# Kernel optimization log

Hardware: AMD Instinct MI355X
Metric: run time of the kernel (lower is better)

## Reference

```python
import jax, jax.numpy as jnp
import numpy as np

B, T_IN, T_OUT = 256, 256, 32
E, H, Y, V = 512, 1024, 1024, 32000


def gru_cell(x, h, Wih, Whh, bih, bhh):
    # torch GRU gate order: r, z, n
    gi = x @ Wih.T + bih
    gh = h @ Whh.T + bhh
    ir, iz, inn = jnp.split(gi, 3, axis=-1)
    hr, hz, hn = jnp.split(gh, 3, axis=-1)
    r = jax.nn.sigmoid(ir + hr)
    z = jax.nn.sigmoid(iz + hz)
    n = jnp.tanh(inn + r * hn)
    return (1.0 - z) * n + z * h


def setup_inputs() -> dict:
    key = jax.random.key(0)
    ks = jax.random.split(key, 32)
    s = 0.05
    p = lambda k, shape: (jax.random.normal(k, shape, jnp.float32) * s)
    inp = {
        'x': jax.random.randint(ks[0], (B, T_IN), 0, V),
        'y': (jax.random.uniform(ks[1], (B, T_OUT, Y)) < 0.01).astype(jnp.float32),
        'emb': p(ks[2], (V, E)),
        # encoder layer 0 (input E) and layer 1 (input H)
        'enc_Wih0': p(ks[3], (3 * H, E)), 'enc_Whh0': p(ks[4], (3 * H, H)),
        'enc_bih0': p(ks[5], (3 * H,)), 'enc_bhh0': p(ks[6], (3 * H,)),
        'enc_Wih1': p(ks[7], (3 * H, H)), 'enc_Whh1': p(ks[8], (3 * H, H)),
        'enc_bih1': p(ks[9], (3 * H,)), 'enc_bhh1': p(ks[10], (3 * H,)),
        # decoder layer 0 (input Y) and layer 1 (input H)
        'dec_Wih0': p(ks[11], (3 * H, Y)), 'dec_Whh0': p(ks[12], (3 * H, H)),
        'dec_bih0': p(ks[13], (3 * H,)), 'dec_bhh0': p(ks[14], (3 * H,)),
        'dec_Wih1': p(ks[15], (3 * H, H)), 'dec_Whh1': p(ks[16], (3 * H, H)),
        'dec_bih1': p(ks[17], (3 * H,)), 'dec_bhh1': p(ks[18], (3 * H,)),
        # mapping: Linear(2H -> Y) followed by log-softmax
        'map_W': p(ks[19], (Y, 2 * H)), 'map_b': p(ks[20], (Y,)),
    }
    return inp


def reference(x, y, emb,
              enc_Wih0, enc_Whh0, enc_bih0, enc_bhh0,
              enc_Wih1, enc_Whh1, enc_bih1, enc_bhh1,
              dec_Wih0, dec_Whh0, dec_bih0, dec_bhh0,
              dec_Wih1, dec_Whh1, dec_bih1, dec_bhh1,
              map_W, map_b):
    batch = x.shape[0]
    h_dim = enc_Whh0.shape[1]

    # ---- encoder: 2-layer GRU over seq_in, h0 = 0 ----
    seq = emb[x].transpose(1, 0, 2)  # [T_in, B, E]
    finals = []
    for prm in ((enc_Wih0, enc_Whh0, enc_bih0, enc_bhh0),
                (enc_Wih1, enc_Whh1, enc_bih1, enc_bhh1)):
        def step(h, xt, prm=prm):
            hn = gru_cell(xt, h, *prm)
            return hn, hn
        hT, seq = jax.lax.scan(step, jnp.zeros((batch, h_dim), seq.dtype), seq)
        finals.append(hT)
    enc_out = seq.transpose(1, 0, 2)  # [B, T_in, H]

    # ---- decoder: teacher-forced, one step at a time ----
    y_shift = jnp.concatenate([jnp.zeros((batch, 1, y.shape[2]), y.dtype), y[:, :-1]], axis=1)
    ys_in = y_shift.transpose(1, 0, 2)  # [T_out, B, Y]
    ys_t = y.transpose(1, 0, 2)         # [T_out, B, Y]
    dec0 = (dec_Wih0, dec_Whh0, dec_bih0, dec_bhh0)
    dec1 = (dec_Wih1, dec_Whh1, dec_bih1, dec_bhh1)

    def dec_step(carry, inp):
        h1, h2 = carry
        y_in, y_t = inp
        h1 = gru_cell(y_in, h1, *dec0)
        h2 = gru_cell(h1, h2, *dec1)           # dec_out == top-layer hidden
        scores = jnp.einsum('bsh,bh->bs', enc_out, h2)
        alpha = jax.nn.softmax(scores, axis=-1)          # over encoder positions
        attn = jnp.einsum('bsh,bs->bh', enc_out, alpha)  # [B, H]
        logits = jnp.concatenate([attn, h2], axis=1) @ map_W.T + map_b
        logp = jax.nn.log_softmax(logits, axis=-1)
        loss_t = -(logp * y_t).sum()
        return (h1, h2), loss_t

    _, losses = jax.lax.scan(dec_step, (finals[0], finals[1]), (ys_in, ys_t))
    return losses.sum() / y.sum()
```

## Files before the change

kernel.cpp:

```cpp
#include <hip/hip_runtime.h>
#include <hip/hip_bf16.h>
#include <math.h>

#define BATCH 256
#define T_IN 256
#define T_OUT 32
#define E_DIM 512
#define H_DIM 1024
#define Y_DIM 1024
#define G_DIM 3072

typedef __attribute__((ext_vector_type(8))) __bf16 bf16x8;
typedef __attribute__((ext_vector_type(4))) float f32x4;
typedef __attribute__((ext_vector_type(4))) unsigned int u32x4;

__device__ __forceinline__ unsigned short f2bf_raw(float x) {
    unsigned int u = __builtin_bit_cast(unsigned int, x);
    u += 0x7FFFu + ((u >> 16) & 1u);
    return (unsigned short)(u >> 16);
}

__global__ __launch_bounds__(256) void f32_to_bf16(
    const float* __restrict__ src, short* __restrict__ dst, int n4)
{
    for (int i = blockIdx.x * 256 + threadIdx.x; i < n4; i += gridDim.x * 256) {
        float4 f = *(const float4*)(src + 4 * (size_t)i);
        short4 o;
        o.x = (short)f2bf_raw(f.x);
        o.y = (short)f2bf_raw(f.y);
        o.z = (short)f2bf_raw(f.z);
        o.w = (short)f2bf_raw(f.w);
        *(short4*)(dst + 4 * (size_t)i) = o;
    }
}

__global__ __launch_bounds__(256) void gemm_bf(
    const short* __restrict__ Ab0, const float* __restrict__ Af0,
    const int* __restrict__ g0, int gs0, int lda0, int K0,
    const short* __restrict__ W0, const float* __restrict__ b0, float* __restrict__ C0,
    const short* __restrict__ Ab1, const float* __restrict__ Af1,
    int lda1, int K1,
    const short* __restrict__ W1, const float* __restrict__ b1, float* __restrict__ C1,
    int N)
{
    const int z = blockIdx.z;
    const short* Ab = z ? Ab1 : Ab0;
    const float* Af = z ? Af1 : Af0;
    const int* gat = z ? nullptr : g0;
    const int gs = z ? 1 : gs0;
    const int lda = z ? lda1 : lda0;
    const int K = z ? K1 : K0;
    const short* W = z ? W1 : W0;
    const float* bias = z ? b1 : b0;
    float* C = z ? C1 : C0;

    __shared__ __align__(16) short As[64 * 40];
    __shared__ __align__(16) short Ws[64 * 40];

    const int tid = threadIdx.x;
    const int bm = blockIdx.x * 64;
    const int bn = blockIdx.y * 64;

    const int srow = tid >> 2;
    const int sch = tid & 3;

    const short* abase = nullptr;
    const float* afbase = nullptr;
    if (Ab) {
        int ridx = gat ? gat[(size_t)(bm + srow) * gs] : (bm + srow);
        abase = Ab + (size_t)ridx * lda;
    } else if (Af) {
        int ridx = gat ? gat[(size_t)(bm + srow) * gs] : (bm + srow);
        afbase = Af + (size_t)ridx * lda;
    }
    const short* wbase = W + (size_t)(bn + srow) * K;

    short* asdst = &As[srow * 40 + sch * 8];
    short* wsdst = &Ws[srow * 40 + sch * 8];

    const int w = tid >> 6;
    const int lane = tid & 63;
    const int wm = (w >> 1) * 32;
    const int wn = (w & 1) * 32;
    const int lrow = lane & 15;
    const int lko = (lane >> 4) * 8;

    const short* ar0 = &As[(wm + lrow) * 40 + lko];
    const short* ar1 = &As[(wm + 16 + lrow) * 40 + lko];
    const short* br0 = &Ws[(wn + lrow) * 40 + lko];
    const short* br1 = &Ws[(wn + 16 + lrow) * 40 + lko];

    f32x4 acc00 = {0.f, 0.f, 0.f, 0.f};
    f32x4 acc01 = acc00, acc10 = acc00, acc11 = acc00;

    for (int k0 = 0; k0 < K; k0 += 32) {
        u32x4 av;
        if (abase) {
            av = *(const u32x4*)(abase + k0 + sch * 8);
        } else if (afbase) {
            const float* fp = afbase + k0 + sch * 8;
            float4 f0 = *(const float4*)(fp);
            float4 f1 = *(const float4*)(fp + 4);
            av.x = ((unsigned)f2bf_raw(f0.y) << 16) | f2bf_raw(f0.x);
            av.y = ((unsigned)f2bf_raw(f0.w) << 16) | f2bf_raw(f0.z);
            av.z = ((unsigned)f2bf_raw(f1.y) << 16) | f2bf_raw(f1.x);
            av.w = ((unsigned)f2bf_raw(f1.w) << 16) | f2bf_raw(f1.z);
        } else {
            av.x = av.y = av.z = av.w = 0u;
        }
        u32x4 wv = *(const u32x4*)(wbase + k0 + sch * 8);
        *(u32x4*)asdst = av;
        *(u32x4*)wsdst = wv;
        __syncthreads();

        bf16x8 a0 = __builtin_bit_cast(bf16x8, *(const u32x4*)ar0);
        bf16x8 a1 = __builtin_bit_cast(bf16x8, *(const u32x4*)ar1);
        bf16x8 b0v = __builtin_bit_cast(bf16x8, *(const u32x4*)br0);
        bf16x8 b1v = __builtin_bit_cast(bf16x8, *(const u32x4*)br1);

        acc00 = __builtin_amdgcn_mfma_f32_16x16x32_bf16(a0, b0v, acc00, 0, 0, 0);
        acc01 = __builtin_amdgcn_mfma_f32_16x16x32_bf16(a0, b1v, acc01, 0, 0, 0);
        acc10 = __builtin_amdgcn_mfma_f32_16x16x32_bf16(a1, b0v, acc10, 0, 0, 0);
        acc11 = __builtin_amdgcn_mfma_f32_16x16x32_bf16(a1, b1v, acc11, 0, 0, 0);

        __syncthreads();
    }

    const int rbase = (lane >> 4) * 4;
    const int cl = lane & 15;
    #pragma unroll
    for (int fm = 0; fm < 2; ++fm) {
        #pragma unroll
        for (int fn = 0; fn < 2; ++fn) {
            f32x4 a = fm ? (fn ? acc11 : acc10) : (fn ? acc01 : acc00);
            int col = bn + wn + fn * 16 + cl;
            float bv = bias[col];
            #pragma unroll
            for (int j = 0; j < 4; ++j) {
                int row = bm + wm + fm * 16 + rbase + j;
                C[(size_t)row * N + col] = a[j] + bv;
            }
        }
    }
}

__global__ __launch_bounds__(256) void gru_fuse(
    const float* __restrict__ gi, const float* __restrict__ gh,
    const float* __restrict__ h, float* __restrict__ hout,
    short* __restrict__ hbf, short* __restrict__ copy_out)
{
    int i = blockIdx.x * 256 + threadIdx.x;
    int b = i >> 10;
    int j = i & 1023;
    const float* gib = gi + (size_t)b * G_DIM;
    const float* ghb = gh + (size_t)b * G_DIM;
    float ir = gib[j], iz = gib[H_DIM + j], in_ = gib[2 * H_DIM + j];
    float hr = ghb[j], hz = ghb[H_DIM + j], hn = ghb[2 * H_DIM + j];
    float r = 1.f / (1.f + expf(-(ir + hr)));
    float zz = 1.f / (1.f + expf(-(iz + hz)));
    float n = tanhf(in_ + r * hn);
    float hv = h[i];
    float o = (1.f - zz) * n + zz * hv;
    hout[i] = o;
    short ob = (short)f2bf_raw(o);
    hbf[i] = ob;
    if (copy_out) copy_out[i] = ob;
}

__global__ __launch_bounds__(256) void attn_scores(
    const short* __restrict__ enc, const float* __restrict__ h2,
    float* __restrict__ scores)
{
    int wid = (blockIdx.x * 256 + threadIdx.x) >> 6;
    int lane = threadIdx.x & 63;
    int s = wid >> 8;
    int b = wid & 255;
    const unsigned int* e2 =
        (const unsigned int*)(enc + ((size_t)s * BATCH + b) * H_DIM);
    const float* hb = h2 + (size_t)b * H_DIM;
    float sum = 0.f;
    #pragma unroll
    for (int p = lane; p < H_DIM / 2; p += 64) {
        unsigned int u = e2[p];
        float lo = __builtin_bit_cast(float, u << 16);
        float hi = __builtin_bit_cast(float, u & 0xFFFF0000u);
        sum += lo * hb[2 * p] + hi * hb[2 * p + 1];
    }
    for (int off = 32; off; off >>= 1) sum += __shfl_down(sum, off);
    if (!lane) scores[(size_t)b * T_IN + s] = sum;
}

__global__ __launch_bounds__(256) void softmax_rows(float* __restrict__ scores)
{
    int b = blockIdx.x, t = threadIdx.x;
    float v = scores[(size_t)b * T_IN + t];
    int lane = t & 63, w = t >> 6;
    float m = v;
    for (int off = 32; off; off >>= 1) m = fmaxf(m, __shfl_down(m, off));
    __shared__ float r1[4];
    if (!lane) r1[w] = m;
    __syncthreads();
    m = fmaxf(fmaxf(r1[0], r1[1]), fmaxf(r1[2], r1[3]));
    float ex = expf(v - m);
    float s = ex;
    for (int off = 32; off; off >>= 1) s += __shfl_down(s, off);
    __shared__ float r2[4];
    if (!lane) r2[w] = s;
    __syncthreads();
    s = r2[0] + r2[1] + r2[2] + r2[3];
    scores[(size_t)b * T_IN + t] = ex / s;
}

__global__ __launch_bounds__(256) void attn_apply(
    const short* __restrict__ enc, const float* __restrict__ alpha,
    float* __restrict__ attn)
{
    int b = blockIdx.x, t = threadIdx.x;
    float acc[4] = {0.f, 0.f, 0.f, 0.f};
    for (int s = 0; s < T_IN; ++s) {
        float a = alpha[(size_t)b * T_IN + s];
        const short* e = enc + ((size_t)s * BATCH + b) * H_DIM;
        #pragma unroll
        for (int i = 0; i < 4; ++i) {
            unsigned int u = ((unsigned int)(unsigned short)e[t + i * 256]) << 16;
            acc[i] += a * __builtin_bit_cast(float, u);
        }
    }
    #pragma unroll
    for (int i = 0; i < 4; ++i) attn[(size_t)b * H_DIM + t + i * 256] = acc[i];
}

__global__ __launch_bounds__(256) void concat_kernel(
    const float* __restrict__ attn, const float* __restrict__ h2,
    short* __restrict__ cat)
{
    int i = blockIdx.x * 256 + threadIdx.x;
    int b = i >> 11;
    int j = i & 2047;
    float v = (j < H_DIM) ? attn[(size_t)b * H_DIM + j]
                          : h2[(size_t)b * H_DIM + j - H_DIM];
    cat[i] = (short)f2bf_raw(v);
}

__global__ __launch_bounds__(256) void loss_kernel(
    const float* __restrict__ logits, const float* __restrict__ yt,
    float* __restrict__ loss_acc)
{
    int b = blockIdx.x, t = threadIdx.x;
    const float* lrow = logits + (size_t)b * Y_DIM;
    float l[4];
    #pragma unroll
    for (int i = 0; i < 4; ++i) l[i] = lrow[t + i * 256];
    float m = fmaxf(fmaxf(l[0], l[1]), fmaxf(l[2], l[3]));
    int lane = t & 63, w = t >> 6;
    for (int off = 32; off; off >>= 1) m = fmaxf(m, __shfl_down(m, off));
    __shared__ float sm[4];
    if (!lane) sm[w] = m;
    __syncthreads();
    m = fmaxf(fmaxf(sm[0], sm[1]), fmaxf(sm[2], sm[3]));
    float es = 0.f;
    #pragma unroll
    for (int i = 0; i < 4; ++i) es += expf(l[i] - m);
    for (int off = 32; off; off >>= 1) es += __shfl_down(es, off);
    __shared__ float ss[4];
    if (!lane) ss[w] = es;
    __syncthreads();
    float sum = ss[0] + ss[1] + ss[2] + ss[3];
    float logZ = m + logf(sum);
    const float* yrow = yt + (size_t)b * (T_OUT * Y_DIM);
    float part = 0.f;
    #pragma unroll
    for (int i = 0; i < 4; ++i) part += yrow[t + i * 256] * (logZ - l[i]);
    for (int off = 32; off; off >>= 1) part += __shfl_down(part, off);
    __shared__ float sp[4];
    if (!lane) sp[w] = part;
    __syncthreads();
    if (t == 0) atomicAdd(loss_acc, sp[0] + sp[1] + sp[2] + sp[3]);
}

__global__ __launch_bounds__(256) void ysum_kernel(
    const float* __restrict__ y, float* __restrict__ ysum, int n)
{
    float s = 0.f;
    for (int i = blockIdx.x * 256 + threadIdx.x; i < n; i += gridDim.x * 256)
        s += y[i];
    int lane = threadIdx.x & 63, w = threadIdx.x >> 6;
    for (int off = 32; off; off >>= 1) s += __shfl_down(s, off);
    __shared__ float sw[4];
    if (!lane) sw[w] = s;
    __syncthreads();
    if (!threadIdx.x) atomicAdd(ysum, sw[0] + sw[1] + sw[2] + sw[3]);
}

__global__ __launch_bounds__(256) void init_kernel(
    float* __restrict__ h0, float* __restrict__ h1,
    short* __restrict__ h0bf, short* __restrict__ h1bf,
    float* __restrict__ loss, float* __restrict__ ysum)
{
    int i = blockIdx.x * 256 + threadIdx.x;
    if (i < BATCH * H_DIM) {
        h0[i] = 0.f; h1[i] = 0.f; h0bf[i] = 0; h1bf[i] = 0;
    }
    if (i == 0) { *loss = 0.f; *ysum = 0.f; }
}

__global__ void final_kernel(const float* __restrict__ loss,
                             const float* __restrict__ ysum,
                             float* __restrict__ out)
{
    if (threadIdx.x == 0) out[0] = loss[0] / ysum[0];
}

extern "C" void kernel_launch(void* const* d_in, const int* in_sizes, int n_in,
                              void* d_out, int out_size, void* d_ws, size_t ws_size,
                              hipStream_t stream)
{
    const int*   x     = (const int*)d_in[0];
    const float* y     = (const float*)d_in[1];
    const float* emb   = (const float*)d_in[2];
    const float* eWih0 = (const float*)d_in[3];
    const float* eWhh0 = (const float*)d_in[4];
    const float* ebih0 = (const float*)d_in[5];
    const float* ebhh0 = (const float*)d_in[6];
    const float* eWih1 = (const float*)d_in[7];
    const float* eWhh1 = (const float*)d_in[8];
    const float* ebih1 = (const float*)d_in[9];
    const float* ebhh1 = (const float*)d_in[10];
    const float* dWih0 = (const float*)d_in[11];
    const float* dWhh0 = (const float*)d_in[12];
    const float* dbih0 = (const float*)d_in[13];
    const float* dbhh0 = (const float*)d_in[14];
    const float* dWih1 = (const float*)d_in[15];
    const float* dWhh1 = (const float*)d_in[16];
    const float* dbih1 = (const float*)d_in[17];
    const float* dbhh1 = (const float*)d_in[18];
    const float* mapW  = (const float*)d_in[19];
    const float* mapb  = (const float*)d_in[20];
    float* out = (float*)d_out;

    char* p = (char*)d_ws;
    short* enc_bf = (short*)p;               p += (size_t)T_IN * BATCH * H_DIM * 2;
    short* eWih0b = (short*)p;               p += (size_t)G_DIM * E_DIM * 2;
    short* eWhh0b = (short*)p;               p += (size_t)G_DIM * H_DIM * 2;
    short* eWih1b = (short*)p;               p += (size_t)G_DIM * H_DIM * 2;
    short* eWhh1b = (short*)p;               p += (size_t)G_DIM * H_DIM * 2;
    short* dWih0b = (short*)p;               p += (size_t)G_DIM * Y_DIM * 2;
    short* dWhh0b = (short*)p;               p += (size_t)G_DIM * H_DIM * 2;
    short* dWih1b = (short*)p;               p += (size_t)G_DIM * H_DIM * 2;
    short* dWhh1b = (short*)p;               p += (size_t)G_DIM * H_DIM * 2;
    short* mapWb  = (short*)p;               p += (size_t)Y_DIM * 2 * H_DIM * 2;
    float* gi0 = (float*)p;                  p += (size_t)BATCH * G_DIM * 4;
    float* gh0 = (float*)p;                  p += (size_t)BATCH * G_DIM * 4;
    float* gi1 = (float*)p;                  p += (size_t)BATCH * G_DIM * 4;
    float* gh1 = (float*)p;                  p += (size_t)BATCH * G_DIM * 4;
    float* h0  = (float*)p;                  p += (size_t)BATCH * H_DIM * 4;
    float* h1  = (float*)p;                  p += (size_t)BATCH * H_DIM * 4;
    short* h0bf = (short*)p;                 p += (size_t)BATCH * H_DIM * 2;
    short* h1bf = (short*)p;                 p += (size_t)BATCH * H_DIM * 2;
    float* scores = (float*)p;               p += (size_t)BATCH * T_IN * 4;
    float* attn   = (float*)p;               p += (size_t)BATCH * H_DIM * 4;
    short* cat_bf = (short*)p;               p += (size_t)BATCH * 2 * H_DIM * 2;
    float* logits = (float*)p;               p += (size_t)BATCH * Y_DIM * 4;
    float* loss_acc = (float*)p;             p += 8;
    float* ysum = loss_acc + 1;

    dim3 blk(256);

    f32_to_bf16<<<dim3(512), blk, 0, stream>>>(eWih0, eWih0b, G_DIM * E_DIM / 4);
    f32_to_bf16<<<dim3(512), blk, 0, stream>>>(eWhh0, eWhh0b, G_DIM * H_DIM / 4);
    f32_to_bf16<<<dim3(512), blk, 0, stream>>>(eWih1, eWih1b, G_DIM * H_DIM / 4);
    f32_to_bf16<<<dim3(512), blk, 0, stream>>>(eWhh1, eWhh1b, G_DIM * H_DIM / 4);
    f32_to_bf16<<<dim3(512), blk, 0, stream>>>(dWih0, dWih0b, G_DIM * Y_DIM / 4);
    f32_to_bf16<<<dim3(512), blk, 0, stream>>>(dWhh0, dWhh0b, G_DIM * H_DIM / 4);
    f32_to_bf16<<<dim3(512), blk, 0, stream>>>(dWih1, dWih1b, G_DIM * H_DIM / 4);
    f32_to_bf16<<<dim3(512), blk, 0, stream>>>(dWhh1, dWhh1b, G_DIM * H_DIM / 4);
    f32_to_bf16<<<dim3(512), blk, 0, stream>>>(mapW, mapWb, Y_DIM * 2 * H_DIM / 4);

    init_kernel<<<dim3(1024), blk, 0, stream>>>(h0, h1, h0bf, h1bf, loss_acc, ysum);
    ysum_kernel<<<dim3(2048), blk, 0, stream>>>(y, ysum, BATCH * T_OUT * Y_DIM);

    dim3 gGate(BATCH / 64, G_DIM / 64, 2);

    for (int t = 0; t < T_IN; ++t) {
        gemm_bf<<<gGate, blk, 0, stream>>>(
            nullptr, emb, x + t, T_IN, E_DIM, E_DIM, eWih0b, ebih0, gi0,
            h0bf, nullptr, H_DIM, H_DIM, eWhh0b, ebhh0, gh0, G_DIM);
        gru_fuse<<<dim3(1024), blk, 0, stream>>>(gi0, gh0, h0, h0, h0bf, nullptr);
        gemm_bf<<<gGate, blk, 0, stream>>>(
            h0bf, nullptr, nullptr, 1, H_DIM, H_DIM, eWih1b, ebih1, gi1,
            h1bf, nullptr, H_DIM, H_DIM, eWhh1b, ebhh1, gh1, G_DIM);
        gru_fuse<<<dim3(1024), blk, 0, stream>>>(
            gi1, gh1, h1, h1, h1bf, enc_bf + (size_t)t * BATCH * H_DIM);
    }

    for (int t = 0; t < T_OUT; ++t) {
        const float* yin = (t == 0) ? nullptr : (y + (size_t)(t - 1) * Y_DIM);
        gemm_bf<<<gGate, blk, 0, stream>>>(
            nullptr, yin, nullptr, 1, T_OUT * Y_DIM, Y_DIM, dWih0b, dbih0, gi0,
            h0bf, nullptr, H_DIM, H_DIM, dWhh0b, dbhh0, gh0, G_DIM);
        gru_fuse<<<dim3(1024), blk, 0, stream>>>(gi0, gh0, h0, h0, h0bf, nullptr);
        gemm_bf<<<gGate, blk, 0, stream>>>(
            h0bf, nullptr, nullptr, 1, H_DIM, H_DIM, dWih1b, dbih1, gi1,
            h1bf, nullptr, H_DIM, H_DIM, dWhh1b, dbhh1, gh1, G_DIM);
        gru_fuse<<<dim3(1024), blk, 0, stream>>>(gi1, gh1, h1, h1, h1bf, nullptr);

        attn_scores<<<dim3(T_IN * BATCH / 4), blk, 0, stream>>>(enc_bf, h1, scores);
        softmax_rows<<<dim3(BATCH), blk, 0, stream>>>(scores);
        attn_apply<<<dim3(BATCH), blk, 0, stream>>>(enc_bf, scores, attn);
        concat_kernel<<<dim3(2048), blk, 0, stream>>>(attn, h1, cat_bf);

        dim3 gMap(BATCH / 64, Y_DIM / 64, 1);
        gemm_bf<<<gMap, blk, 0, stream>>>(
            cat_bf, nullptr, nullptr, 1, 2 * H_DIM, 2 * H_DIM, mapWb, mapb, logits,
            nullptr, nullptr, 0, 0, nullptr, nullptr, nullptr, Y_DIM);
        loss_kernel<<<dim3(BATCH), blk, 0, stream>>>(
            logits, y + (size_t)t * Y_DIM, loss_acc);
    }

    final_kernel<<<dim3(1), dim3(64), 0, stream>>>(loss_acc, ysum, out);
}
```

Measured before the change: 15.23 ms.

## Fuse GRU gate GEMMs with cell update, wavefront-pipeline layers, batch decoder attention

```diff
diff --git a/kernel.cpp b/kernel.cpp
--- a/kernel.cpp
+++ b/kernel.cpp
@@ -18,6 +18,16 @@
     unsigned int u = __builtin_bit_cast(unsigned int, x);
     u += 0x7FFFu + ((u >> 16) & 1u);
     return (unsigned short)(u >> 16);
+}
+__device__ __forceinline__ float bf2f(short s) {
+    unsigned int u = ((unsigned int)(unsigned short)s) << 16;
+    return __builtin_bit_cast(float, u);
+}
+__device__ __forceinline__ f32x4 mfma16(bf16x8 a, bf16x8 b, f32x4 c) {
+    return __builtin_amdgcn_mfma_f32_16x16x32_bf16(a, b, c, 0, 0, 0);
+}
+__device__ __forceinline__ bf16x8 ldsb8(const short* p) {
+    return __builtin_bit_cast(bf16x8, *(const u32x4*)p);
 }
 
 __global__ __launch_bounds__(256) void f32_to_bf16(
@@ -34,166 +44,179 @@
     }
 }
 
-__global__ __launch_bounds__(256) void gemm_bf(
-    const short* __restrict__ Ab0, const float* __restrict__ Af0,
-    const int* __restrict__ g0, int gs0, int lda0, int K0,
-    const short* __restrict__ W0, const float* __restrict__ b0, float* __restrict__ C0,
-    const short* __restrict__ Ab1, const float* __restrict__ Af1,
-    int lda1, int K1,
-    const short* __restrict__ W1, const float* __restrict__ b1, float* __restrict__ C1,
-    int N)
-{
-    const int z = blockIdx.z;
-    const short* Ab = z ? Ab1 : Ab0;
-    const float* Af = z ? Af1 : Af0;
-    const int* gat = z ? nullptr : g0;
-    const int gs = z ? 1 : gs0;
-    const int lda = z ? lda1 : lda0;
-    const int K = z ? K1 : K0;
-    const short* W = z ? W1 : W0;
-    const float* bias = z ? b1 : b0;
-    float* C = z ? C1 : C0;
-
-    __shared__ __align__(16) short As[64 * 40];
-    __shared__ __align__(16) short Ws[64 * 40];
+struct CellArgs {
+    const float* Af; const short* Ab; const int* gat; int gs; int lda; int Kx;
+    const short* Wih; const short* Whh;
+    const float* bih; const float* bhh;
+    const short* hbf;
+    const float* hf;
+    float* houtf; short* houtbf; short* copy;
+    int active;
+};
+
+__global__ __launch_bounds__(256) void cell_kernel(CellArgs cA, CellArgs cB)
+{
+    const CellArgs a = blockIdx.z ? cB : cA;
+    if (!a.active) return;
+
+    __shared__ __align__(16) short As[2 * 1280];
+    __shared__ __align__(16) short Ws[6 * 2560];
 
     const int tid = threadIdx.x;
-    const int bm = blockIdx.x * 64;
+    const int bm = blockIdx.x * 32;
     const int bn = blockIdx.y * 64;
 
-    const int srow = tid >> 2;
-    const int sch = tid & 3;
-
-    const short* abase = nullptr;
-    const float* afbase = nullptr;
-    if (Ab) {
-        int ridx = gat ? gat[(size_t)(bm + srow) * gs] : (bm + srow);
-        abase = Ab + (size_t)ridx * lda;
-    } else if (Af) {
-        int ridx = gat ? gat[(size_t)(bm + srow) * gs] : (bm + srow);
-        afbase = Af + (size_t)ridx * lda;
-    }
-    const short* wbase = W + (size_t)(bn + srow) * K;
-
-    short* asdst = &As[srow * 40 + sch * 8];
-    short* wsdst = &Ws[srow * 40 + sch * 8];
-
+    const int sr = (tid >> 2) & 31;
+    const int ss = tid >> 7;
+    const int wr = tid >> 2;
+    const int ch = (tid & 3) * 8;
+
+    const float* axf = nullptr;
+    const short* axb = nullptr;
+    if (a.Af) {
+        int ridx = a.gat ? a.gat[(size_t)(bm + sr) * a.gs] : (bm + sr);
+        axf = a.Af + (size_t)ridx * a.lda + ch;
+    } else if (a.Ab) {
+        axb = a.Ab + (size_t)(bm + sr) * a.lda + ch;
+    }
+    const short* ahb = a.hbf + (size_t)(bm + sr) * H_DIM + ch;
+
+    const short* wsrc[6];
+    #pragma unroll
+    for (int g = 0; g < 3; ++g) {
+        wsrc[g]     = a.Wih + (size_t)(g * H_DIM + bn + wr) * a.Kx + ch;
+        wsrc[g + 3] = a.Whh + (size_t)(g * H_DIM + bn + wr) * H_DIM + ch;
+    }
+    short* adst  = &As[ss * 1280 + sr * 40 + ch];
+    short* wdst0 = &Ws[wr * 40 + ch];
+
+    const int lane = tid & 63;
     const int w = tid >> 6;
-    const int lane = tid & 63;
-    const int wm = (w >> 1) * 32;
-    const int wn = (w & 1) * 32;
-    const int lrow = lane & 15;
-    const int lko = (lane >> 4) * 8;
-
-    const short* ar0 = &As[(wm + lrow) * 40 + lko];
-    const short* ar1 = &As[(wm + 16 + lrow) * 40 + lko];
-    const short* br0 = &Ws[(wn + lrow) * 40 + lko];
-    const short* br1 = &Ws[(wn + 16 + lrow) * 40 + lko];
-
-    f32x4 acc00 = {0.f, 0.f, 0.f, 0.f};
-    f32x4 acc01 = acc00, acc10 = acc00, acc11 = acc00;
-
-    for (int k0 = 0; k0 < K; k0 += 32) {
-        u32x4 av;
-        if (abase) {
-            av = *(const u32x4*)(abase + k0 + sch * 8);
-        } else if (afbase) {
-            const float* fp = afbase + k0 + sch * 8;
-            float4 f0 = *(const float4*)(fp);
-            float4 f1 = *(const float4*)(fp + 4);
-            av.x = ((unsigned)f2bf_raw(f0.y) << 16) | f2bf_raw(f0.x);
-            av.y = ((unsigned)f2bf_raw(f0.w) << 16) | f2bf_raw(f0.z);
-            av.z = ((unsigned)f2bf_raw(f1.y) << 16) | f2bf_raw(f1.x);
-            av.w = ((unsigned)f2bf_raw(f1.w) << 16) | f2bf_raw(f1.z);
-        } else {
-            av.x = av.y = av.z = av.w = 0u;
-        }
-        u32x4 wv = *(const u32x4*)(wbase + k0 + sch * 8);
-        *(u32x4*)asdst = av;
-        *(u32x4*)wsdst = wv;
+    const int lr = lane & 15;
+    const int ko = (lane >> 4) * 8;
+    const short* pax0 = &As[lr * 40 + ko];
+    const short* pax1 = &As[(16 + lr) * 40 + ko];
+    const short* pah0 = &As[1280 + lr * 40 + ko];
+    const short* pah1 = &As[1280 + (16 + lr) * 40 + ko];
+    const int wc = (w * 16 + lr) * 40 + ko;
+
+    f32x4 accI[3][2] = {{{0.f,0.f,0.f,0.f}}};
+    f32x4 accH[3][2] = {{{0.f,0.f,0.f,0.f}}};
+
+    const int Kx = a.Kx;
+    for (int k0 = 0; k0 < H_DIM; k0 += 32) {
+        const bool xact = (k0 < Kx);
+        u32x4 av = {0u, 0u, 0u, 0u};
+        if (ss) {
+            av = *(const u32x4*)(ahb + k0);
+        } else if (xact) {
+            if (axb) {
+                av = *(const u32x4*)(axb + k0);
+            } else if (axf) {
+                float4 f0 = *(const float4*)(axf + k0);
+                float4 f1 = *(const float4*)(axf + k0 + 4);
+                av.x = ((unsigned)f2bf_raw(f0.y) << 16) | f2bf_raw(f0.x);
+                av.y = ((unsigned)f2bf_raw(f0.w) << 16) | f2bf_raw(f0.z);
+                av.z = ((unsigned)f2bf_raw(f1.y) << 16) | f2bf_raw(f1.x);
+                av.w = ((unsigned)f2bf_raw(f1.w) << 16) | f2bf_raw(f1.z);
+            }
+        }
+        if (ss || xact) *(u32x4*)adst = av;
+        #pragma unroll
+        for (int i = 0; i < 6; ++i) {
+            if (i >= 3 || xact)
+                *(u32x4*)(wdst0 + i * 2560) = *(const u32x4*)(wsrc[i] + k0);
+        }
         __syncthreads();
-
-        bf16x8 a0 = __builtin_bit_cast(bf16x8, *(const u32x4*)ar0);
-        bf16x8 a1 = __builtin_bit_cast(bf16x8, *(const u32x4*)ar1);
-        bf16x8 b0v = __builtin_bit_cast(bf16x8, *(const u32x4*)br0);
-        bf16x8 b1v = __builtin_bit_cast(bf16x8, *(const u32x4*)br1);
-
-        acc00 = __builtin_amdgcn_mfma_f32_16x16x32_bf16(a0, b0v, acc00, 0, 0, 0);
-        acc01 = __builtin_amdgcn_mfma_f32_16x16x32_bf16(a0, b1v, acc01, 0, 0, 0);
-        acc10 = __builtin_amdgcn_mfma_f32_16x16x32_bf16(a1, b0v, acc10, 0, 0, 0);
-        acc11 = __builtin_amdgcn_mfma_f32_16x16x32_bf16(a1, b1v, acc11, 0, 0, 0);
-
+        bf16x8 ah0 = ldsb8(pah0), ah1 = ldsb8(pah1);
+        #pragma unroll
+        for (int g = 0; g < 3; ++g) {
+            bf16x8 wh = ldsb8(&Ws[(g + 3) * 2560 + wc]);
+            accH[g][0] = mfma16(ah0, wh, accH[g][0]);
+            accH[g][1] = mfma16(ah1, wh, accH[g][1]);
+        }
+        if (xact) {
+            bf16x8 ax0 = ldsb8(pax0), ax1 = ldsb8(pax1);
+            #pragma unroll
+            for (int g = 0; g < 3; ++g) {
+                bf16x8 wi = ldsb8(&Ws[g * 2560 + wc]);
+                accI[g][0] = mfma16(ax0, wi, accI[g][0]);
+                accI[g][1] = mfma16(ax1, wi, accI[g][1]);
+            }
+        }
         __syncthreads();
     }
 
-    const int rbase = (lane >> 4) * 4;
-    const int cl = lane & 15;
-    #pragma unroll
-    for (int fm = 0; fm < 2; ++fm) {
-        #pragma unroll
-        for (int fn = 0; fn < 2; ++fn) {
-            f32x4 a = fm ? (fn ? acc11 : acc10) : (fn ? acc01 : acc00);
-            int col = bn + wn + fn * 16 + cl;
-            float bv = bias[col];
-            #pragma unroll
-            for (int j = 0; j < 4; ++j) {
-                int row = bm + wm + fm * 16 + rbase + j;
-                C[(size_t)row * N + col] = a[j] + bv;
-            }
-        }
-    }
-}
-
-__global__ __launch_bounds__(256) void gru_fuse(
-    const float* __restrict__ gi, const float* __restrict__ gh,
-    const float* __restrict__ h, float* __restrict__ hout,
-    short* __restrict__ hbf, short* __restrict__ copy_out)
-{
-    int i = blockIdx.x * 256 + threadIdx.x;
-    int b = i >> 10;
-    int j = i & 1023;
-    const float* gib = gi + (size_t)b * G_DIM;
-    const float* ghb = gh + (size_t)b * G_DIM;
-    float ir = gib[j], iz = gib[H_DIM + j], in_ = gib[2 * H_DIM + j];
-    float hr = ghb[j], hz = ghb[H_DIM + j], hn = ghb[2 * H_DIM + j];
-    float r = 1.f / (1.f + expf(-(ir + hr)));
-    float zz = 1.f / (1.f + expf(-(iz + hz)));
-    float n = tanhf(in_ + r * hn);
-    float hv = h[i];
-    float o = (1.f - zz) * n + zz * hv;
-    hout[i] = o;
-    short ob = (short)f2bf_raw(o);
-    hbf[i] = ob;
-    if (copy_out) copy_out[i] = ob;
-}
-
-__global__ __launch_bounds__(256) void attn_scores(
-    const short* __restrict__ enc, const float* __restrict__ h2,
-    float* __restrict__ scores)
-{
-    int wid = (blockIdx.x * 256 + threadIdx.x) >> 6;
-    int lane = threadIdx.x & 63;
-    int s = wid >> 8;
-    int b = wid & 255;
-    const unsigned int* e2 =
-        (const unsigned int*)(enc + ((size_t)s * BATCH + b) * H_DIM);
-    const float* hb = h2 + (size_t)b * H_DIM;
-    float sum = 0.f;
-    #pragma unroll
-    for (int p = lane; p < H_DIM / 2; p += 64) {
-        unsigned int u = e2[p];
-        float lo = __builtin_bit_cast(float, u << 16);
-        float hi = __builtin_bit_cast(float, u & 0xFFFF0000u);
-        sum += lo * hb[2 * p] + hi * hb[2 * p + 1];
-    }
-    for (int off = 32; off; off >>= 1) sum += __shfl_down(sum, off);
-    if (!lane) scores[(size_t)b * T_IN + s] = sum;
-}
-
-__global__ __launch_bounds__(256) void softmax_rows(float* __restrict__ scores)
-{
-    int b = blockIdx.x, t = threadIdx.x;
-    float v = scores[(size_t)b * T_IN + t];
+    const int j = bn + w * 16 + lr;
+    const float bi0 = a.bih[j], bi1 = a.bih[H_DIM + j], bi2 = a.bih[2 * H_DIM + j];
+    const float bh0 = a.bhh[j], bh1 = a.bhh[H_DIM + j], bh2 = a.bhh[2 * H_DIM + j];
+    #pragma unroll
+    for (int rh = 0; rh < 2; ++rh) {
+        #pragma unroll
+        for (int q = 0; q < 4; ++q) {
+            int row = bm + rh * 16 + (lane >> 4) * 4 + q;
+            float ir = accI[0][rh][q] + bi0, hr = accH[0][rh][q] + bh0;
+            float iz = accI[1][rh][q] + bi1, hz = accH[1][rh][q] + bh1;
+            float in_ = accI[2][rh][q] + bi2, hn = accH[2][rh][q] + bh2;
+            float r = 1.f / (1.f + expf(-(ir + hr)));
+            float z = 1.f / (1.f + expf(-(iz + hz)));
+            float n = tanhf(in_ + r * hn);
+            size_t oi = (size_t)row * H_DIM + j;
+            float hv = a.hf[oi];
+            float o = (1.f - z) * n + z * hv;
+            a.houtf[oi] = o;
+            short ob = (short)f2bf_raw(o);
+            a.houtbf[oi] = ob;
+            if (a.copy) a.copy[oi] = ob;
+        }
+    }
+}
+
+__global__ __launch_bounds__(256) void score_gemm(
+    const short* __restrict__ h2all, const short* __restrict__ enc,
+    float* __restrict__ S)
+{
+    const int st = blockIdx.x;
+    const int b = blockIdx.y;
+    __shared__ __align__(16) short Hs[32 * 40];
+    __shared__ __align__(16) short Es[64 * 40];
+    const int tid = threadIdx.x;
+    const int ch = (tid & 3) * 8;
+    const int hrow = (tid >> 2) & 31;
+    const int erow = tid >> 2;
+    const short* hsrc = h2all + ((size_t)hrow * BATCH + b) * H_DIM + ch;
+    const short* esrc = enc + ((size_t)(st * 64 + erow) * BATCH + b) * H_DIM + ch;
+    short* hdst = &Hs[hrow * 40 + ch];
+    short* edst = &Es[erow * 40 + ch];
+
+    const int lane = tid & 63, w = tid >> 6;
+    const int lr = lane & 15, ko = (lane >> 4) * 8;
+    f32x4 acc0 = {0.f, 0.f, 0.f, 0.f}, acc1 = acc0;
+    for (int k0 = 0; k0 < H_DIM; k0 += 32) {
+        if (tid < 128) *(u32x4*)hdst = *(const u32x4*)(hsrc + k0);
+        *(u32x4*)edst = *(const u32x4*)(esrc + k0);
+        __syncthreads();
+        bf16x8 e = ldsb8(&Es[(w * 16 + lr) * 40 + ko]);
+        bf16x8 h0v = ldsb8(&Hs[lr * 40 + ko]);
+        bf16x8 h1v = ldsb8(&Hs[(16 + lr) * 40 + ko]);
+        acc0 = mfma16(h0v, e, acc0);
+        acc1 = mfma16(h1v, e, acc1);
+        __syncthreads();
+    }
+    int s = st * 64 + w * 16 + lr;
+    #pragma unroll
+    for (int q = 0; q < 4; ++q) {
+        int t0 = (lane >> 4) * 4 + q;
+        S[(size_t)b * 8192 + (size_t)t0 * 256 + s] = acc0[q];
+        S[(size_t)b * 8192 + (size_t)(t0 + 16) * 256 + s] = acc1[q];
+    }
+}
+
+__global__ __launch_bounds__(256) void softmax_all(float* __restrict__ S)
+{
+    size_t base = (size_t)blockIdx.x * 256;
+    int t = threadIdx.x;
+    float v = S[base + t];
     int lane = t & 63, w = t >> 6;
     float m = v;
     for (int off = 32; off; off >>= 1) m = fmaxf(m, __shfl_down(m, off));
@@ -208,66 +231,125 @@
     if (!lane) r2[w] = s;
     __syncthreads();
     s = r2[0] + r2[1] + r2[2] + r2[3];
-    scores[(size_t)b * T_IN + t] = ex / s;
-}
-
-__global__ __launch_bounds__(256) void attn_apply(
-    const short* __restrict__ enc, const float* __restrict__ alpha,
-    float* __restrict__ attn)
-{
-    int b = blockIdx.x, t = threadIdx.x;
-    float acc[4] = {0.f, 0.f, 0.f, 0.f};
-    for (int s = 0; s < T_IN; ++s) {
-        float a = alpha[(size_t)b * T_IN + s];
-        const short* e = enc + ((size_t)s * BATCH + b) * H_DIM;
-        #pragma unroll
-        for (int i = 0; i < 4; ++i) {
-            unsigned int u = ((unsigned int)(unsigned short)e[t + i * 256]) << 16;
-            acc[i] += a * __builtin_bit_cast(float, u);
-        }
-    }
-    #pragma unroll
-    for (int i = 0; i < 4; ++i) attn[(size_t)b * H_DIM + t + i * 256] = acc[i];
-}
-
-__global__ __launch_bounds__(256) void concat_kernel(
-    const float* __restrict__ attn, const float* __restrict__ h2,
-    short* __restrict__ cat)
-{
-    int i = blockIdx.x * 256 + threadIdx.x;
-    int b = i >> 11;
-    int j = i & 2047;
-    float v = (j < H_DIM) ? attn[(size_t)b * H_DIM + j]
-                          : h2[(size_t)b * H_DIM + j - H_DIM];
-    cat[i] = (short)f2bf_raw(v);
-}
-
-__global__ __launch_bounds__(256) void loss_kernel(
-    const float* __restrict__ logits, const float* __restrict__ yt,
+    S[base + t] = ex / s;
+}
+
+__global__ __launch_bounds__(256) void attn_apply_all(
+    const short* __restrict__ enc, const float* __restrict__ S,
+    short* __restrict__ attn_bf)
+{
+    const int tc = blockIdx.x, b = blockIdx.y;
+    __shared__ float al[8][256];
+    const int tid = threadIdx.x;
+    #pragma unroll
+    for (int ti = 0; ti < 8; ++ti)
+        al[ti][tid] = S[(size_t)b * 8192 + (size_t)(tc * 8 + ti) * 256 + tid];
+    __syncthreads();
+    float acc[8][4] = {};
+    const short* eb = enc + (size_t)b * H_DIM + tid;
+    for (int s = 0; s < 256; ++s) {
+        const short* er = eb + (size_t)s * (BATCH * H_DIM);
+        float e0 = bf2f(er[0]), e1 = bf2f(er[256]);
+        float e2 = bf2f(er[512]), e3 = bf2f(er[768]);
+        #pragma unroll
+        for (int ti = 0; ti < 8; ++ti) {
+            float av = al[ti][s];
+            acc[ti][0] += av * e0; acc[ti][1] += av * e1;
+            acc[ti][2] += av * e2; acc[ti][3] += av * e3;
+        }
+    }
+    #pragma unroll
+    for (int ti = 0; ti < 8; ++ti) {
+        size_t m = (size_t)(tc * 8 + ti) * 256 + b;
+        #pragma unroll
+        for (int i = 0; i < 4; ++i)
+            attn_bf[m * H_DIM + tid + i * 256] = (short)f2bf_raw(acc[ti][i]);
+    }
+}
+
+__global__ __launch_bounds__(256) void map_gemm(
+    const short* __restrict__ A1, const short* __restrict__ A2,
+    const short* __restrict__ Wm, const float* __restrict__ bias,
+    float* __restrict__ C)
+{
+    const int bm = blockIdx.x * 64, bn = blockIdx.y * 64;
+    __shared__ __align__(16) short S1[64 * 40], S2[64 * 40], T1[64 * 40], T2[64 * 40];
+    const int tid = threadIdx.x;
+    const int r = tid >> 2, ch = (tid & 3) * 8;
+    const short* a1 = A1 + (size_t)(bm + r) * 1024 + ch;
+    const short* a2 = A2 + (size_t)(bm + r) * 1024 + ch;
+    const short* w1 = Wm + (size_t)(bn + r) * 2048 + ch;
+    const short* w2 = w1 + 1024;
+    const int lane = tid & 63, w = tid >> 6;
+    const int wm = (w >> 1) * 32, wn = (w & 1) * 32;
+    const int lr = lane & 15, ko = (lane >> 4) * 8;
+    f32x4 acc[2][2] = {{{0.f,0.f,0.f,0.f}}};
+    for (int k0 = 0; k0 < 1024; k0 += 32) {
+        *(u32x4*)&S1[r * 40 + ch] = *(const u32x4*)(a1 + k0);
+        *(u32x4*)&S2[r * 40 + ch] = *(const u32x4*)(a2 + k0);
+        *(u32x4*)&T1[r * 40 + ch] = *(const u32x4*)(w1 + k0);
+        *(u32x4*)&T2[r * 40 + ch] = *(const u32x4*)(w2 + k0);
+        __syncthreads();
+        bf16x8 x1[2], x2[2], y1[2], y2[2];
+        #pragma unroll
+        for (int i = 0; i < 2; ++i) {
+            x1[i] = ldsb8(&S1[(wm + i * 16 + lr) * 40 + ko]);
+            x2[i] = ldsb8(&S2[(wm + i * 16 + lr) * 40 + ko]);
+            y1[i] = ldsb8(&T1[(wn + i * 16 + lr) * 40 + ko]);
+            y2[i] = ldsb8(&T2[(wn + i * 16 + lr) * 40 + ko]);
+        }
+        #pragma unroll
+        for (int i = 0; i < 2; ++i) {
+            #pragma unroll
+            for (int jq = 0; jq < 2; ++jq) {
+                acc[i][jq] = mfma16(x1[i], y1[jq], acc[i][jq]);
+                acc[i][jq] = mfma16(x2[i], y2[jq], acc[i][jq]);
+            }
+        }
+        __syncthreads();
+    }
+    #pragma unroll
+    for (int i = 0; i < 2; ++i) {
+        #pragma unroll
+        for (int jq = 0; jq < 2; ++jq) {
+            int col = bn + wn + jq * 16 + lr;
+            float bv = bias[col];
+            #pragma unroll
+            for (int q = 0; q < 4; ++q) {
+                int row = bm + wm + i * 16 + (lane >> 4) * 4 + q;
+                C[(size_t)row * 1024 + col] = acc[i][jq][q] + bv;
+            }
+        }
+    }
+}
+
+__global__ __launch_bounds__(256) void loss_all(
+    const float* __restrict__ logits, const float* __restrict__ y,
     float* __restrict__ loss_acc)
 {
-    int b = blockIdx.x, t = threadIdx.x;
-    const float* lrow = logits + (size_t)b * Y_DIM;
+    int m = blockIdx.x, t = threadIdx.x;
+    int tt = m >> 8, b = m & 255;
+    const float* lrow = logits + (size_t)m * Y_DIM;
     float l[4];
     #pragma unroll
     for (int i = 0; i < 4; ++i) l[i] = lrow[t + i * 256];
-    float m = fmaxf(fmaxf(l[0], l[1]), fmaxf(l[2], l[3]));
+    float mx = fmaxf(fmaxf(l[0], l[1]), fmaxf(l[2], l[3]));
     int lane = t & 63, w = t >> 6;
-    for (int off = 32; off; off >>= 1) m = fmaxf(m, __shfl_down(m, off));
+    for (int off = 32; off; off >>= 1) mx = fmaxf(mx, __shfl_down(mx, off));
     __shared__ float sm[4];
-    if (!lane) sm[w] = m;
-    __syncthreads();
-    m = fmaxf(fmaxf(sm[0], sm[1]), fmaxf(sm[2], sm[3]));
+    if (!lane) sm[w] = mx;
+    __syncthreads();
+    mx = fmaxf(fmaxf(sm[0], sm[1]), fmaxf(sm[2], sm[3]));
     float es = 0.f;
     #pragma unroll
-    for (int i = 0; i < 4; ++i) es += expf(l[i] - m);
+    for (int i = 0; i < 4; ++i) es += expf(l[i] - mx);
     for (int off = 32; off; off >>= 1) es += __shfl_down(es, off);
     __shared__ float ss[4];
     if (!lane) ss[w] = es;
     __syncthreads();
     float sum = ss[0] + ss[1] + ss[2] + ss[3];
-    float logZ = m + logf(sum);
-    const float* yrow = yt + (size_t)b * (T_OUT * Y_DIM);
+    float logZ = mx + logf(sum);
+    const float* yrow = y + ((size_t)b * T_OUT + tt) * Y_DIM;
     float part = 0.f;
     #pragma unroll
     for (int i = 0; i < 4; ++i) part += yrow[t + i * 256] * (logZ - l[i]);
@@ -294,13 +376,11 @@
 
 __global__ __launch_bounds__(256) void init_kernel(
     float* __restrict__ h0, float* __restrict__ h1,
-    short* __restrict__ h0bf, short* __restrict__ h1bf,
+    short* __restrict__ h0b, short* __restrict__ h1b,
     float* __restrict__ loss, float* __restrict__ ysum)
 {
     int i = blockIdx.x * 256 + threadIdx.x;
-    if (i < BATCH * H_DIM) {
-        h0[i] = 0.f; h1[i] = 0.f; h0bf[i] = 0; h1bf[i] = 0;
-    }
+    h0[i] = 0.f; h1[i] = 0.f; h0b[i] = 0; h1b[i] = 0;
     if (i == 0) { *loss = 0.f; *ysum = 0.f; }
 }
 
@@ -339,30 +419,31 @@
     float* out = (float*)d_out;
 
     char* p = (char*)d_ws;
-    short* enc_bf = (short*)p;               p += (size_t)T_IN * BATCH * H_DIM * 2;
-    short* eWih0b = (short*)p;               p += (size_t)G_DIM * E_DIM * 2;
-    short* eWhh0b = (short*)p;               p += (size_t)G_DIM * H_DIM * 2;
-    short* eWih1b = (short*)p;               p += (size_t)G_DIM * H_DIM * 2;
-    short* eWhh1b = (short*)p;               p += (size_t)G_DIM * H_DIM * 2;
-    short* dWih0b = (short*)p;               p += (size_t)G_DIM * Y_DIM * 2;
-    short* dWhh0b = (short*)p;               p += (size_t)G_DIM * H_DIM * 2;
-    short* dWih1b = (short*)p;               p += (size_t)G_DIM * H_DIM * 2;
-    short* dWhh1b = (short*)p;               p += (size_t)G_DIM * H_DIM * 2;
-    short* mapWb  = (short*)p;               p += (size_t)Y_DIM * 2 * H_DIM * 2;
-    float* gi0 = (float*)p;                  p += (size_t)BATCH * G_DIM * 4;
-    float* gh0 = (float*)p;                  p += (size_t)BATCH * G_DIM * 4;
-    float* gi1 = (float*)p;                  p += (size_t)BATCH * G_DIM * 4;
-    float* gh1 = (float*)p;                  p += (size_t)BATCH * G_DIM * 4;
-    float* h0  = (float*)p;                  p += (size_t)BATCH * H_DIM * 4;
-    float* h1  = (float*)p;                  p += (size_t)BATCH * H_DIM * 4;
-    short* h0bf = (short*)p;                 p += (size_t)BATCH * H_DIM * 2;
-    short* h1bf = (short*)p;                 p += (size_t)BATCH * H_DIM * 2;
-    float* scores = (float*)p;               p += (size_t)BATCH * T_IN * 4;
-    float* attn   = (float*)p;               p += (size_t)BATCH * H_DIM * 4;
-    short* cat_bf = (short*)p;               p += (size_t)BATCH * 2 * H_DIM * 2;
-    float* logits = (float*)p;               p += (size_t)BATCH * Y_DIM * 4;
-    float* loss_acc = (float*)p;             p += 8;
+    auto take = [&](size_t n) { char* q = p; p += (n + 255) & ~(size_t)255; return q; };
+    short* enc_bf = (short*)take((size_t)T_IN * BATCH * H_DIM * 2);
+    char* wslab = p;
+    short* eWih0b = (short*)take((size_t)G_DIM * E_DIM * 2);
+    short* eWhh0b = (short*)take((size_t)G_DIM * H_DIM * 2);
+    short* eWih1b = (short*)take((size_t)G_DIM * H_DIM * 2);
+    short* eWhh1b = (short*)take((size_t)G_DIM * H_DIM * 2);
+    short* dWih0b = (short*)take((size_t)G_DIM * Y_DIM * 2);
+    short* dWhh0b = (short*)take((size_t)G_DIM * H_DIM * 2);
+    short* dWih1b = (short*)take((size_t)G_DIM * H_DIM * 2);
+    short* dWhh1b = (short*)take((size_t)G_DIM * H_DIM * 2);
+    short* mapWb  = (short*)take((size_t)Y_DIM * 2 * H_DIM * 2);
+    float* h0f[2]; float* h1f[2]; short* h0b[2]; short* h1b[2];
+    for (int i = 0; i < 2; ++i) {
+        h0f[i] = (float*)take((size_t)BATCH * H_DIM * 4);
+        h1f[i] = (float*)take((size_t)BATCH * H_DIM * 4);
+        h0b[i] = (short*)take((size_t)BATCH * H_DIM * 2);
+        h1b[i] = (short*)take((size_t)BATCH * H_DIM * 2);
+    }
+    short* h2all = (short*)take((size_t)T_OUT * BATCH * H_DIM * 2);
+    float* loss_acc = (float*)take(256);
     float* ysum = loss_acc + 1;
+    float* logits  = (float*)enc_bf;
+    short* attn_bf = (short*)wslab;
+    float* S       = (float*)(wslab + (size_t)20 * 1024 * 1024);
 
     dim3 blk(256);
 
@@ -376,46 +457,58 @@
     f32_to_bf16<<<dim3(512), blk, 0, stream>>>(dWhh1, dWhh1b, G_DIM * H_DIM / 4);
     f32_to_bf16<<<dim3(512), blk, 0, stream>>>(mapW, mapWb, Y_DIM * 2 * H_DIM / 4);
 
-    init_kernel<<<dim3(1024), blk, 0, stream>>>(h0, h1, h0bf, h1bf, loss_acc, ysum);
+    init_kernel<<<dim3(BATCH * H_DIM / 256), blk, 0, stream>>>(
+        h0f[0], h1f[0], h0b[0], h1b[0], loss_acc, ysum);
     ysum_kernel<<<dim3(2048), blk, 0, stream>>>(y, ysum, BATCH * T_OUT * Y_DIM);
 
-    dim3 gGate(BATCH / 64, G_DIM / 64, 2);
-
-    for (int t = 0; t < T_IN; ++t) {
-        gemm_bf<<<gGate, blk, 0, stream>>>(
-            nullptr, emb, x + t, T_IN, E_DIM, E_DIM, eWih0b, ebih0, gi0,
-            h0bf, nullptr, H_DIM, H_DIM, eWhh0b, ebhh0, gh0, G_DIM);
-        gru_fuse<<<dim3(1024), blk, 0, stream>>>(gi0, gh0, h0, h0, h0bf, nullptr);
-        gemm_bf<<<gGate, blk, 0, stream>>>(
-            h0bf, nullptr, nullptr, 1, H_DIM, H_DIM, eWih1b, ebih1, gi1,
-            h1bf, nullptr, H_DIM, H_DIM, eWhh1b, ebhh1, gh1, G_DIM);
-        gru_fuse<<<dim3(1024), blk, 0, stream>>>(
-            gi1, gh1, h1, h1, h1bf, enc_bf + (size_t)t * BATCH * H_DIM);
-    }
-
-    for (int t = 0; t < T_OUT; ++t) {
-        const float* yin = (t == 0) ? nullptr : (y + (size_t)(t - 1) * Y_DIM);
-        gemm_bf<<<gGate, blk, 0, stream>>>(
-            nullptr, yin, nullptr, 1, T_OUT * Y_DIM, Y_DIM, dWih0b, dbih0, gi0,
-            h0bf, nullptr, H_DIM, H_DIM, dWhh0b, dbhh0, gh0, G_DIM);
-        gru_fuse<<<dim3(1024), blk, 0, stream>>>(gi0, gh0, h0, h0, h0bf, nullptr);
-        gemm_bf<<<gGate, blk, 0, stream>>>(
-            h0bf, nullptr, nullptr, 1, H_DIM, H_DIM, dWih1b, dbih1, gi1,
-            h1bf, nullptr, H_DIM, H_DIM, dWhh1b, dbhh1, gh1, G_DIM);
-        gru_fuse<<<dim3(1024), blk, 0, stream>>>(gi1, gh1, h1, h1, h1bf, nullptr);
-
-        attn_scores<<<dim3(T_IN * BATCH / 4), blk, 0, stream>>>(enc_bf, h1, scores);
-        softmax_rows<<<dim3(BATCH), blk, 0, stream>>>(scores);
-        attn_apply<<<dim3(BATCH), blk, 0, stream>>>(enc_bf, scores, attn);
-        concat_kernel<<<dim3(2048), blk, 0, stream>>>(attn, h1, cat_bf);
-
-        dim3 gMap(BATCH / 64, Y_DIM / 64, 1);
-        gemm_bf<<<gMap, blk, 0, stream>>>(
-            cat_bf, nullptr, nullptr, 1, 2 * H_DIM, 2 * H_DIM, mapWb, mapb, logits,
-            nullptr, nullptr, 0, 0, nullptr, nullptr, nullptr, Y_DIM);
-        loss_kernel<<<dim3(BATCH), blk, 0, stream>>>(
-            logits, y + (size_t)t * Y_DIM, loss_acc);
-    }
+    dim3 gCell(8, 16, 2);
+
+    for (int k = 0; k <= T_IN; ++k) {
+        CellArgs A = {}, B = {};
+        A.active = (k < T_IN);
+        if (A.active) {
+            A.Af = emb; A.gat = x + k; A.gs = T_IN; A.lda = E_DIM; A.Kx = E_DIM;
+            A.Wih = eWih0b; A.Whh = eWhh0b; A.bih = ebih0; A.bhh = ebhh0;
+            A.hbf = h0b[k & 1]; A.hf = h0f[k & 1];
+            A.houtf = h0f[(k + 1) & 1]; A.houtbf = h0b[(k + 1) & 1];
+        }
+        B.active = (k >= 1);
+        if (B.active) {
+            B.Ab = h0b[k & 1]; B.lda = H_DIM; B.Kx = H_DIM;
+            B.Wih = eWih1b; B.Whh = eWhh1b; B.bih = ebih1; B.bhh = ebhh1;
+            B.hbf = h1b[(k - 1) & 1]; B.hf = h1f[(k - 1) & 1];
+            B.houtf = h1f[k & 1]; B.houtbf = h1b[k & 1];
+            B.copy = enc_bf + (size_t)(k - 1) * BATCH * H_DIM;
+        }
+        cell_kernel<<<gCell, blk, 0, stream>>>(A, B);
+    }
+
+    for (int k = 0; k <= T_OUT; ++k) {
+        CellArgs A = {}, B = {};
+        A.active = (k < T_OUT);
+        if (A.active) {
+            A.Af = (k == 0) ? nullptr : (y + (size_t)(k - 1) * Y_DIM);
+            A.lda = T_OUT * Y_DIM; A.Kx = Y_DIM;
+            A.Wih = dWih0b; A.Whh = dWhh0b; A.bih = dbih0; A.bhh = dbhh0;
+            A.hbf = h0b[k & 1]; A.hf = h0f[k & 1];
+            A.houtf = h0f[(k + 1) & 1]; A.houtbf = h0b[(k + 1) & 1];
+        }
+        B.active = (k >= 1);
+        if (B.active) {
+            B.Ab = h0b[k & 1]; B.lda = H_DIM; B.Kx = H_DIM;
+            B.Wih = dWih1b; B.Whh = dWhh1b; B.bih = dbih1; B.bhh = dbhh1;
+            B.hbf = h1b[(k - 1) & 1]; B.hf = h1f[(k - 1) & 1];
+            B.houtf = h1f[k & 1]; B.houtbf = h1b[k & 1];
+            B.copy = h2all + (size_t)(k - 1) * BATCH * H_DIM;
+        }
+        cell_kernel<<<gCell, blk, 0, stream>>>(A, B);
+    }
+
+    score_gemm<<<dim3(4, 256), blk, 0, stream>>>(h2all, enc_bf, S);
+    softmax_all<<<dim3(8192), blk, 0, stream>>>(S);
+    attn_apply_all<<<dim3(4, 256), blk, 0, stream>>>(enc_bf, S, attn_bf);
+    map_gemm<<<dim3(128, 16), blk, 0, stream>>>(attn_bf, h2all, mapWb, mapb, logits);
+    loss_all<<<dim3(8192), blk, 0, stream>>>(logits, y, loss_acc);
 
     final_kernel<<<dim3(1), dim3(64), 0, stream>>>(loss_acc, ysum, out);
 }
```

After: 15.23 ms. No clear change (+0.0%).
